# Optimization experiments

Measured on AMD Instinct MI355X. Metric: run time of the kernel, lower is better.

The kernel has to match this reference:

```python
import jax, jax.numpy as jnp
import numpy as np

DIM = 512
K_ALL = 11
K_TOP = 4
DOMAIN = 10
EPS = 1e-12
NEG_INF = -1e30

def _normalize(x):
    n = jnp.linalg.norm(x, axis=-1, keepdims=True)
    return x / jnp.maximum(n, EPS)

def _leaky(x):
    return jax.nn.leaky_relu(x, 0.01)

def setup_inputs():
    key = jax.random.key(0)
    ks = jax.random.split(key, 16)
    Bp, Lp, Bg, Lg = 128, 256, 64, 512
    probes = jax.random.normal(ks[0], (1, Bp, Lp, DIM), jnp.float32)
    gallery = jax.random.normal(ks[1], (1, Bg, Lg, DIM), jnp.float32)
    probe_lengths = jax.random.randint(ks[2], (1, Bp), 1, Lp + 1)
    gallery_lengths = jax.random.randint(ks[3], (1, Bg), 1, Lg + 1)
    proxies_p = jax.random.normal(ks[4], (K_ALL, DIM), jnp.float32) * 0.06
    proxies_g = jax.random.normal(ks[5], (K_ALL, DIM), jnp.float32) * 0.06
    transform_W = jax.random.normal(ks[6], (DOMAIN, DIM), jnp.float32) * 0.06
    transform_b = jnp.zeros((DOMAIN,), jnp.float32)
    probe_W = jnp.eye(DIM, dtype=jnp.float32)  # nn.init.eye_
    probe_b = jnp.zeros((DIM,), jnp.float32)
    # pooler MLP weights stacked over the 11 experts; init_weights: N(0, 0.001), zero bias
    pool_W1 = jax.random.normal(ks[7], (K_ALL, 2 * DIM, 3 * DIM), jnp.float32) * 1e-3
    pool_b1 = jnp.zeros((K_ALL, 2 * DIM), jnp.float32)
    pool_W2 = jax.random.normal(ks[8], (K_ALL, 2 * DIM, 2 * DIM), jnp.float32) * 1e-3
    pool_b2 = jnp.zeros((K_ALL, 2 * DIM), jnp.float32)
    pool_W3 = jax.random.normal(ks[9], (K_ALL, DIM, 2 * DIM), jnp.float32) * 1e-3
    pool_b3 = jnp.zeros((K_ALL, DIM), jnp.float32)
    return dict(probes=probes, gallery=gallery, probe_lengths=probe_lengths,
                gallery_lengths=gallery_lengths, proxies_p=proxies_p, proxies_g=proxies_g,
                transform_W=transform_W, transform_b=transform_b, probe_W=probe_W,
                probe_b=probe_b, pool_W1=pool_W1, pool_b1=pool_b1, pool_W2=pool_W2,
                pool_b2=pool_b2, pool_W3=pool_W3, pool_b3=pool_b3)

def reference(probes, gallery, probe_lengths, gallery_lengths, proxies_p, proxies_g,
              transform_W, transform_b, probe_W, probe_b,
              pool_W1, pool_b1, pool_W2, pool_b2, pool_W3, pool_b3):
    def fuse(feat, length, proxies, use_probe_linear):
        # feat: [L, D], length: scalar int; masked equivalent of feat[:length]
        L = feat.shape[0]
        fmask = (jnp.arange(L) < length).astype(feat.dtype)[:, None]  # [L, 1]
        lp = jnp.maximum(length, 1).astype(feat.dtype)
        normed = _normalize(feat)
        tf = _normalize(feat @ transform_W.T + transform_b)        # [L, 10]
        tp = _normalize(proxies @ transform_W.T + transform_b)      # [K_ALL, 10]
        sims = tf @ tp.T                                            # [L, K_ALL]
        gsim = (sims * fmask).sum(0)                                # [K_ALL]
        _, idx = jax.lax.top_k(gsim, K_TOP)
        mean = (feat * fmask).sum(0) / lp                           # [D]
        var = (((feat - mean) ** 2) * fmask).sum(0) / lp            # biased variance
        summary = jnp.concatenate([jnp.tile(mean[None], (K_TOP, 1)),
                                   jnp.tile(var[None], (K_TOP, 1)),
                                   proxies[idx]], axis=-1)          # [K_TOP, 3D]
        # expert-gathered pooler MLPs (dropout = identity in eval)
        h = _leaky(jnp.einsum('koi,ki->ko', pool_W1[idx], summary) + pool_b1[idx])
        h = _leaky(jnp.einsum('koi,ki->ko', pool_W2[idx], h) + pool_b2[idx])
        ctx = _leaky(jnp.einsum('koi,ki->ko', pool_W3[idx], h) + pool_b3[idx])  # [K_TOP, D]
        q = feat @ probe_W.T + probe_b if use_probe_linear else feat
        scores = q @ ctx.T                                          # [L, K_TOP]
        scores = jnp.where(fmask > 0, scores, NEG_INF)
        w = jax.nn.softmax(scores, axis=0)                          # softmax over set dim
        return jnp.einsum('ld,lk->kd', normed, w)                   # [K_TOP, D]

    p, g = probes[0], gallery[0]
    pl, gl = probe_lengths[0], gallery_lengths[0]
    final_probe = jax.vmap(lambda f, l: fuse(f, l, proxies_p, True))(p, pl)
    final_gallery = jax.vmap(lambda f, l: fuse(f, l, proxies_g, False))(g, gl)
    return (final_probe,
            proxies_p @ transform_W.T + transform_b,
            final_gallery,
            proxies_g @ transform_W.T + transform_b)
```

## Files before the change

### kernel.cpp

```cpp
#include <hip/hip_runtime.h>
#include <hip/hip_bf16.h>

namespace {

using us = unsigned short;
typedef __attribute__((ext_vector_type(8))) short bf16x8;
typedef __attribute__((ext_vector_type(4))) float f32x4;
typedef __attribute__((ext_vector_type(4))) unsigned short us4;
typedef __attribute__((ext_vector_type(4))) unsigned int u32x4;

constexpr int DIM_ = 512, KALL = 11, DOM = 10, NPROBE = 128, NSETS = 192;
constexpr int LPR = 256, LGA = 512;

constexpr size_t O_OUT1 = 0;
constexpr size_t O_OUT2 = (size_t)NPROBE * 4 * DIM_;
constexpr size_t O_OUT3 = O_OUT2 + KALL * DOM;
constexpr size_t O_OUT4 = O_OUT3 + (size_t)64 * 4 * DIM_;

constexpr size_t F_TP   = 64;
constexpr size_t F_IDX  = 320;
constexpr size_t F_S0A  = 1600;
constexpr size_t F_WQ   = 4096;
constexpr size_t F_GP   = 495616;
constexpr size_t F_SUMM = 514048;
constexpr size_t F_H1   = 612352;
constexpr size_t F_PART = F_H1;
constexpr size_t F_CTXW = F_H1;
constexpr size_t F_H2   = 1693696;
constexpr size_t F_ACC  = F_H2;
constexpr size_t F_CTX  = 2775040;
constexpr size_t F_WT   = 3315712;
constexpr size_t F_BEFF = 3446784;
constexpr size_t WS_FLOATS = F_BEFF + 2 * KALL * 1024;
constexpr size_t WS_BYTES  = WS_FLOATS * 4;

__device__ __forceinline__ float b2f(us u) { return __uint_as_float(((unsigned)u) << 16); }
__device__ __forceinline__ us f2b(float x) {
    unsigned u = __float_as_uint(x);
    u += 0x7FFF + ((u >> 16) & 1);
    return (us)(u >> 16);
}
__device__ __forceinline__ float ldT(const float* p) { return *p; }
__device__ __forceinline__ float ldT(const us* p) { return b2f(*p); }
__device__ __forceinline__ void stT(float* p, float v) { *p = v; }
__device__ __forceinline__ void stT(us* p, float v) { *p = f2b(v); }

__device__ __forceinline__ bf16x8 loadA(const us* p) { return *(const bf16x8*)p; }
__device__ __forceinline__ bf16x8 loadA(const float* p) {
    f32x4 a = *(const f32x4*)p, b = *(const f32x4*)(p + 4);
    bf16x8 r;
#pragma unroll
    for (int j = 0; j < 4; ++j) { r[j] = (short)f2b(a[j]); r[4 + j] = (short)f2b(b[j]); }
    return r;
}
__device__ __forceinline__ bf16x8 pack8(f32x4 a, f32x4 b) {
    bf16x8 r;
#pragma unroll
    for (int j = 0; j < 4; ++j) { r[j] = (short)f2b(a[j]); r[4 + j] = (short)f2b(b[j]); }
    return r;
}

__device__ __forceinline__ void gload_lds16(const us* g, us* l) {
    __builtin_amdgcn_global_load_lds(
        (const __attribute__((address_space(1))) void*)g,
        (__attribute__((address_space(3))) void*)l, 16, 0, 0);
}

__device__ __forceinline__ void decode64(int bx, int& set, int& base, int& L) {
    if (bx < 512) { set = bx >> 2; base = (bx & 3) * 64; L = LPR; }
    else { set = NPROBE + ((bx - 512) >> 3); base = ((bx - 512) & 7) * 64; L = LGA; }
}

__global__ void detect_kernel(const unsigned int* probeW_bits, int* flag) {
    if (threadIdx.x == 0) *flag = (probeW_bits[0] == 0x3F800000u) ? 0 : 1;
}

template <typename T>
__device__ void proxies_body(const T* pp, const T* pg, const T* tW, const T* tb,
                             float* wsf, T* dout) {
    int b = blockIdx.x;
    int fam = b / KALL, i = b % KALL;
    int lane = threadIdx.x;
    const T* src = fam ? pg : pp;
    float t[DOM];
#pragma unroll
    for (int r = 0; r < DOM; ++r) t[r] = 0.f;
    for (int d = lane; d < DIM_; d += 64) {
        float x = ldT(src + (size_t)i * DIM_ + d);
#pragma unroll
        for (int r = 0; r < DOM; ++r) t[r] += x * ldT(tW + (size_t)r * DIM_ + d);
    }
#pragma unroll
    for (int off = 32; off >= 1; off >>= 1)
#pragma unroll
        for (int r = 0; r < DOM; ++r) t[r] += __shfl_xor(t[r], off, 64);
#pragma unroll
    for (int r = 0; r < DOM; ++r) t[r] += ldT(tb + r);
    float nn = 0.f;
#pragma unroll
    for (int r = 0; r < DOM; ++r) nn += t[r] * t[r];
    float inv = 1.0f / fmaxf(sqrtf(nn), 1e-12f);
    if (lane < DOM) {
        size_t base = fam ? O_OUT4 : O_OUT2;
        stT(dout + base + i * DOM + lane, t[lane]);
        wsf[F_TP + fam * 128 + i * DOM + lane] = t[lane] * inv;
    }
}
__global__ void proxies_kernel(const int* flag, const void* pp, const void* pg,
                               const void* tW, const void* tb, float* wsf, void* dout) {
    if (*flag)
        proxies_body<us>((const us*)pp, (const us*)pg, (const us*)tW, (const us*)tb, wsf, (us*)dout);
    else
        proxies_body<float>((const float*)pp, (const float*)pg, (const float*)tW, (const float*)tb, wsf, (float*)dout);
}

template <typename T>
__device__ void pbias_body(const T* W1, const T* b1, const T* pp, const T* pg, float* beff) {
    int bx = blockIdx.x;
    int e = bx >> 4, ch = bx & 15;
    int tid = threadIdx.x;
    int om = tid >> 2, sub = tid & 3;
    int m = ch * 64 + om;
    const T* wr = W1 + ((size_t)e * 1024 + m) * 1536 + 1024 + sub * 128;
    const T* pr = pp + (size_t)e * DIM_ + sub * 128;
    const T* gr = pg + (size_t)e * DIM_ + sub * 128;
    float sp = 0.f, sg = 0.f;
    if constexpr (sizeof(T) == 2) {
#pragma unroll 4
        for (int k = 0; k < 128; k += 2) {
            unsigned wv = *(const unsigned*)(wr + k);
            unsigned pv = *(const unsigned*)(pr + k);
            unsigned gv = *(const unsigned*)(gr + k);
            float w0 = __uint_as_float(wv << 16), w1 = __uint_as_float(wv & 0xFFFF0000u);
            float p0 = __uint_as_float(pv << 16), p1 = __uint_as_float(pv & 0xFFFF0000u);
            float g0 = __uint_as_float(gv << 16), g1 = __uint_as_float(gv & 0xFFFF0000u);
            sp += w0 * p0 + w1 * p1;
            sg += w0 * g0 + w1 * g1;
        }
    } else {
#pragma unroll 2
        for (int k = 0; k < 128; k += 4) {
            f32x4 wv = *(const f32x4*)(wr + k);
            f32x4 pv = *(const f32x4*)(pr + k);
            f32x4 gv = *(const f32x4*)(gr + k);
#pragma unroll
            for (int q = 0; q < 4; ++q) { sp += wv[q] * pv[q]; sg += wv[q] * gv[q]; }
        }
    }
    sp += __shfl_xor(sp, 1, 64); sp += __shfl_xor(sp, 2, 64);
    sg += __shfl_xor(sg, 1, 64); sg += __shfl_xor(sg, 2, 64);
    if (sub == 0) {
        float bb = ldT(b1 + (size_t)e * 1024 + m);
        beff[(size_t)e * 1024 + m] = bb + sp;
        beff[(size_t)(KALL + e) * 1024 + m] = bb + sg;
    }
}
__global__ void pbias_kernel(const int* flag, const void* W1, const void* b1,
                             const void* pp, const void* pg, float* beff) {
    if (*flag)
        pbias_body<us>((const us*)W1, (const us*)b1, (const us*)pp, (const us*)pg, beff);
    else
        pbias_body<float>((const float*)W1, (const float*)b1, (const float*)pp, (const float*)pg, beff);
}

template <typename T>
__device__ void sums_body(const T* probes, const T* gallery, const int* plen,
                          const int* glen, float* wsf) {
    int bx = blockIdx.x, set = bx >> 2, c = bx & 3;
    bool probe = set < NPROBE;
    int L = probe ? LPR : LGA;
    const T* feat = probe ? probes + (size_t)set * L * DIM_
                          : gallery + (size_t)(set - NPROBE) * L * DIM_;
    int len = probe ? plen[set] : glen[set - NPROBE];
    int len_eff = min(max(len, 1), L);
    int r0 = (c * len_eff) >> 2, r1 = ((c + 1) * len_eff) >> 2;
    __shared__ float psum[DIM_], psq[DIM_];
    int tid = threadIdx.x, w = tid >> 6, lane = tid & 63;
    psum[tid] = 0.f; psum[tid + 256] = 0.f;
    psq[tid] = 0.f; psq[tid + 256] = 0.f;
    __syncthreads();
    float asum[8] = {0,0,0,0,0,0,0,0}, asq[8] = {0,0,0,0,0,0,0,0};
    for (int l = r0 + w * 2; l < r1; l += 8) {
        bool two = (l + 1 < r1);
        float f0[8], f1[8];
        if constexpr (sizeof(T) == 2) {
            u32x4 ra = *(const u32x4*)(feat + (size_t)l * DIM_ + lane * 8);
            u32x4 rb = two ? *(const u32x4*)(feat + (size_t)(l + 1) * DIM_ + lane * 8)
                           : (u32x4){0, 0, 0, 0};
#pragma unroll
            for (int q = 0; q < 4; ++q) {
                f0[2*q] = __uint_as_float(ra[q] << 16);
                f0[2*q+1] = __uint_as_float(ra[q] & 0xFFFF0000u);
                f1[2*q] = __uint_as_float(rb[q] << 16);
                f1[2*q+1] = __uint_as_float(rb[q] & 0xFFFF0000u);
            }
        } else {
            const T* rp = feat + (size_t)l * DIM_ + lane * 8;
            f32x4 a0 = *(const f32x4*)rp, a1 = *(const f32x4*)(rp + 4);
#pragma unroll
            for (int j = 0; j < 4; ++j) { f0[j] = a0[j]; f0[4+j] = a1[j]; }
            if (two) {
                const T* rq = feat + (size_t)(l + 1) * DIM_ + lane * 8;
                f32x4 b0 = *(const f32x4*)rq, b1 = *(const f32x4*)(rq + 4);
#pragma unroll
                for (int j = 0; j < 4; ++j) { f1[j] = b0[j]; f1[4+j] = b1[j]; }
            } else {
#pragma unroll
                for (int j = 0; j < 8; ++j) f1[j] = 0.f;
            }
        }
#pragma unroll
        for (int j = 0; j < 8; ++j) {
            asum[j] += f0[j] + f1[j];
            asq[j] += f0[j] * f0[j] + f1[j] * f1[j];
        }
    }
#pragma unroll
    for (int j = 0; j < 8; ++j) {
        atomicAdd(&psum[lane * 8 + j], asum[j]);
        atomicAdd(&psq[lane * 8 + j], asq[j]);
    }
    __syncthreads();
    float* P = wsf + F_PART + (size_t)bx * 1024;
    P[tid] = psum[tid]; P[tid + 256] = psum[tid + 256];
    P[512 + tid] = psq[tid]; P[768 + tid] = psq[tid + 256];
}
__global__ __launch_bounds__(256) void sums_kernel(const int* flag, const void* probes,
        const void* gallery, const int* plen, const int* glen, float* wsf) {
    if (*flag) sums_body<us>((const us*)probes, (const us*)gallery, plen, glen, wsf);
    else sums_body<float>((const float*)probes, (const float*)gallery, plen, glen, wsf);
}

template <typename T>
__device__ void sims_body(const T* probes, const T* gallery, const int* plen,
                          const int* glen, const T* tW, float* wsf) {
    int bx = blockIdx.x, set, base, L;
    decode64(bx, set, base, L);
    bool probe = set < NPROBE;
    int len = probe ? plen[set] : glen[set - NPROBE];
    int len_eff = min(max(len, 1), L);
    float* GP = wsf + F_GP + (size_t)bx * 12;
    int tid = threadIdx.x;
    if (base >= len_eff) { if (tid < KALL) GP[tid] = 0.f; return; }
    const T* feat = probe ? probes + (size_t)set * L * DIM_
                          : gallery + (size_t)(set - NPROBE) * L * DIM_;
    __shared__ __align__(16) float tile[4][320];
    __shared__ float tpl[KALL * DOM];
    __shared__ float gs[16];
    if (tid < KALL * DOM) tpl[tid] = wsf[F_TP + (probe ? 0 : 128) + tid];
    if (tid < 16) gs[tid] = 0.f;
    int w = tid >> 6, lane = tid & 63, lm = lane & 15, quad = lane >> 4;

    bf16x8 bq[16];
#pragma unroll
    for (int s = 0; s < 16; ++s) {
        if (lm < DOM) bq[s] = loadA(tW + (size_t)lm * DIM_ + s * 32 + quad * 8);
        else bq[s] = (bf16x8){0, 0, 0, 0, 0, 0, 0, 0};
    }
    int m0 = base + w * 16;
    const T* Ap = feat + (size_t)(m0 + lm) * DIM_ + quad * 8;
    f32x4 acc = (f32x4){0.f, 0.f, 0.f, 0.f};
    float vsq = 0.f;
#pragma unroll
    for (int s = 0; s < 16; ++s) {
        bf16x8 a;
        if constexpr (sizeof(T) == 2) {
            a = *(const bf16x8*)(Ap + s * 32);
#pragma unroll
            for (int j = 0; j < 8; ++j) { float x = b2f((us)a[j]); vsq += x * x; }
        } else {
            f32x4 p0 = *(const f32x4*)(Ap + s * 32), p1 = *(const f32x4*)(Ap + s * 32 + 4);
#pragma unroll
            for (int j = 0; j < 4; ++j) {
                vsq += p0[j] * p0[j] + p1[j] * p1[j];
                a[j] = (short)f2b(p0[j]); a[4 + j] = (short)f2b(p1[j]);
            }
        }
        acc = __builtin_amdgcn_mfma_f32_16x16x32_bf16(a, bq[s], acc, 0, 0, 0);
    }
    vsq += __shfl_xor(vsq, 16, 64);
    vsq += __shfl_xor(vsq, 32, 64);
    {
        int rown = m0 + lm;
        if (quad == 0 && rown < len_eff)
            wsf[F_WQ + (size_t)set * 2560 + (size_t)rown * 5 + 4] =
                1.0f / fmaxf(sqrtf(vsq), 1e-12f);
    }
#pragma unroll
    for (int r = 0; r < 4; ++r) tile[w][(quad * 4 + r) * 20 + lm] = acc[r];
    __syncthreads();

    float gacc[KALL];
#pragma unroll
    for (int k = 0; k < KALL; ++k) gacc[k] = 0.f;
    if (lane < 16) {
        int row = m0 + lane;
        if (row < len_eff) {
            const float* tr = &tile[w][lane * 20];
            f32x4 t0 = *(const f32x4*)tr, t1 = *(const f32x4*)(tr + 4);
            float tv[DOM] = {t0[0], t0[1], t0[2], t0[3], t1[0], t1[1], t1[2], t1[3], tr[8], tr[9]};
            float nn = 0.f;
#pragma unroll
            for (int r = 0; r < DOM; ++r) nn += tv[r] * tv[r];
            float inv = 1.0f / fmaxf(sqrtf(nn), 1e-12f);
#pragma unroll
            for (int k = 0; k < KALL; ++k) {
                float s = 0.f;
#pragma unroll
                for (int r = 0; r < DOM; ++r) s += tv[r] * tpl[k * DOM + r];
                gacc[k] = s * inv;
            }
        }
    }
#pragma unroll
    for (int off = 8; off >= 1; off >>= 1)
#pragma unroll
        for (int k = 0; k < KALL; ++k) gacc[k] += __shfl_xor(gacc[k], off, 64);
    if (lane == 0)
#pragma unroll
        for (int k = 0; k < KALL; ++k) atomicAdd(&gs[k], gacc[k]);
    __syncthreads();
    if (tid < KALL) GP[tid] = gs[tid];
}
__global__ __launch_bounds__(256, 3) void sims_kernel(const int* flag, const void* probes,
        const void* gallery, const int* plen, const int* glen, const void* tW, float* wsf) {
    if (*flag) sims_body<us>((const us*)probes, (const us*)gallery, plen, glen, (const us*)tW, wsf);
    else sims_body<float>((const float*)probes, (const float*)gallery, plen, glen, (const float*)tW, wsf);
}

__global__ void statsfin_kernel(const int* plen, const int* glen, float* wsf) {
    int set = blockIdx.x, tid = threadIdx.x;
    bool probe = set < NPROBE;
    int len = probe ? plen[set] : glen[set - NPROBE];
    float lp = (float)max(len, 1);
    const float* P = wsf + F_PART + (size_t)set * 4 * 1024;
    us* SUMM = (us*)(wsf + F_SUMM);
    for (int d = tid; d < DIM_; d += 256) {
        float s = P[d] + P[1024 + d] + P[2048 + d] + P[3072 + d];
        float q = P[512 + d] + P[1536 + d] + P[2560 + d] + P[3584 + d];
        float m = s / lp;
        float v = q / lp - m * m;
        SUMM[(size_t)set * 1024 + d] = f2b(m);
        SUMM[(size_t)set * 1024 + DIM_ + d] = f2b(v);
    }
    if (tid == 0) {
        int nch = probe ? 4 : 8;
        int gb = probe ? set * 4 : 512 + (set - NPROBE) * 8;
        float g[KALL];
        for (int i = 0; i < KALL; ++i) {
            float s = 0.f;
            for (int c = 0; c < nch; ++c) s += wsf[F_GP + (size_t)(gb + c) * 12 + i];
            g[i] = s;
        }
        int* idx4 = (int*)(wsf + F_IDX);
        for (int kk = 0; kk < 4; ++kk) {
            int bi = 0; float bv = g[0];
            for (int i = 1; i < KALL; ++i)
                if (g[i] > bv) { bv = g[i]; bi = i; }
            idx4[set * 4 + kk] = bi;
            g[bi] = -3e38f;
        }
    }
}

template <typename T>
__device__ void wt_body(const T* W, us* WT) {
    __shared__ us t[64][65];
    int bi = blockIdx.y * 64, bj = blockIdx.x * 64, tid = threadIdx.x;
    for (int i = tid; i < 4096; i += 256) {
        int r = i >> 6, cc = i & 63;
        t[r][cc] = (sizeof(T) == 2) ? ((const us*)W)[(size_t)(bi + r) * DIM_ + bj + cc]
                                    : f2b(ldT(W + (size_t)(bi + r) * DIM_ + bj + cc));
    }
    __syncthreads();
    for (int i = tid; i < 4096; i += 256) {
        int r = i >> 6, cc = i & 63;
        WT[(size_t)(bj + r) * DIM_ + bi + cc] = t[cc][r];
    }
}
__global__ void wt_kernel(const int* flag, const void* W, us* WT) {
    if (*flag) wt_body<us>((const us*)W, WT);
    else wt_body<float>((const float*)W, WT);
}

template <int M, int KS, int L1>
__global__ __launch_bounds__(256) void mlp_one(const int* flag, const void* Wv,
        const void* biasv, const us* X, us* Y, const float* beff) {
    constexpr int MT = M / 64;
    constexpr int NK = 16;
    int flagv = *flag;
    __shared__ us SM[8192];
    int bx = blockIdx.x;
    int nt = bx / (MT * KALL);
    int rem = bx - nt * (MT * KALL);
    int e = rem % KALL;
    int mt = rem / KALL;
    int tid = threadIdx.x, w = tid >> 6, lane = tid & 63;
    int lm = lane & 15, quad = lane >> 4;
    int s0 = nt * 64;
    const size_t aoff = ((size_t)e * M + mt * 64 + w * 16 + lm) * KS + quad * 8;
    const float* AF = (const float*)Wv + aoff;
    const us*    AB = (const us*)Wv + aoff;
    int xrow0 = (L1 ? 0 : e * NSETS) + s0;
    int slot0 = w * 64 + lane, slot1 = slot0 + 256;
    int brow0 = slot0 >> 3, bcol0 = (slot0 & 7) ^ (brow0 & 7);
    int brow1 = slot1 >> 3, bcol1 = (slot1 & 7) ^ (brow1 & 7);
    const us* Xs0 = X + ((size_t)(xrow0 + brow0)) * 1024 + bcol0 * 8;
    const us* Xs1 = X + ((size_t)(xrow0 + brow1)) * 1024 + bcol1 * 8;
    us* ls0 = SM + slot0 * 8;
    us* ls1 = SM + slot1 * 8;

    f32x4 acc[4];
#pragma unroll
    for (int j = 0; j < 4; ++j) acc[j] = (f32x4){0.f, 0.f, 0.f, 0.f};

    bf16x8 a0[2], a1[2];
    f32x4 pan[4];

    auto issueB = [&](int par, int k0) {
        gload_lds16(Xs0 + k0, ls0 + par * 4096);
        gload_lds16(Xs1 + k0, ls1 + par * 4096);
    };
    auto loadAx = [&](int k0, bf16x8* adst) {
        if (flagv) {
            adst[0] = *(const bf16x8*)(AB + k0);
            adst[1] = *(const bf16x8*)(AB + k0 + 32);
        } else {
            pan[0] = *(const f32x4*)(AF + k0);
            pan[1] = *(const f32x4*)(AF + k0 + 4);
            pan[2] = *(const f32x4*)(AF + k0 + 32);
            pan[3] = *(const f32x4*)(AF + k0 + 36);
        }
    };
    auto packA = [&](bf16x8* adst) {
        if (!flagv) {
            adst[0] = pack8(pan[0], pan[1]);
            adst[1] = pack8(pan[2], pan[3]);
        }
    };
    auto compute = [&](int par, const bf16x8* a) {
        const us* Bb = SM + par * 4096;
#pragma unroll
        for (int ks = 0; ks < 2; ++ks)
#pragma unroll
            for (int j = 0; j < 4; ++j) {
                int br = j * 16 + lm;
                int cg = ks * 4 + quad;
                bf16x8 b = *(const bf16x8*)(Bb + br * 64 + ((cg ^ (br & 7)) * 8));
                acc[j] = __builtin_amdgcn_mfma_f32_16x16x32_bf16(a[ks], b, acc[j], 0, 0, 0);
            }
    };

    issueB(0, 0);
    loadAx(0, a0);
    packA(a0);
    __syncthreads();
#pragma unroll 1
    for (int t = 0; t < NK; t += 2) {
        int k1 = (t + 1) * 64, k2 = (t + 2) * 64;
        if (t + 1 < NK) { issueB(1, k1); loadAx(k1, a1); }
        compute(0, a0);
        if (t + 1 < NK) packA(a1);
        __syncthreads();
        if (t + 1 < NK) {
            if (t + 2 < NK) { issueB(0, k2); loadAx(k2, a0); }
            compute(1, a1);
            if (t + 2 < NK) packA(a0);
            __syncthreads();
        }
    }

    int m0 = mt * 64 + w * 16 + quad * 4;
    float bv[4];
    if (L1) {
        const float* be = beff + ((size_t)((nt < 2) ? 0 : KALL) + e) * 1024 + m0;
#pragma unroll
        for (int r = 0; r < 4; ++r) bv[r] = be[r];
    } else {
#pragma unroll
        for (int r = 0; r < 4; ++r)
            bv[r] = flagv ? b2f(((const us*)biasv)[(size_t)e * M + m0 + r])
                          : ((const float*)biasv)[(size_t)e * M + m0 + r];
    }
#pragma unroll
    for (int j = 0; j < 4; ++j) {
        int s = s0 + j * 16 + lm;
        us4 pk;
#pragma unroll
        for (int r = 0; r < 4; ++r) {
            float v = acc[j][r] + bv[r];
            v = v > 0.f ? v : 0.01f * v;
            pk[r] = f2b(v);
        }
        *(us4*)(Y + ((size_t)e * NSETS + s) * M + m0) = pk;
    }
}

__global__ void fold_kernel(const us* CTX, const us* WT, us* CTXW) {
    int nt = blockIdx.x, mtb = blockIdx.y;
    int e = mtb >> 1, sub = mtb & 1;
    int row0 = e * NSETS + sub * 64;
    int tid = threadIdx.x, w = tid >> 6, lane = tid & 63;
    int lm = lane & 15, quad = lane >> 4, kq = quad * 8;
    const us* Ap = CTX + ((size_t)row0 + w * 16 + lm) * DIM_ + kq;
    int n0 = nt * 64;
    const us* Bp = WT + (size_t)(n0 + lm) * DIM_ + kq;
    f32x4 acc[4];
#pragma unroll
    for (int j = 0; j < 4; ++j) acc[j] = (f32x4){0.f, 0.f, 0.f, 0.f};
#pragma unroll 2
    for (int kc = 0; kc < DIM_; kc += 32) {
        bf16x8 a = *(const bf16x8*)(Ap + kc);
#pragma unroll
        for (int j = 0; j < 4; ++j) {
            bf16x8 b = *(const bf16x8*)(Bp + kc + (size_t)j * 16 * DIM_);
            acc[j] = __builtin_amdgcn_mfma_f32_16x16x32_bf16(a, b, acc[j], 0, 0, 0);
        }
    }
    int mrow = row0 + w * 16 + quad * 4;
#pragma unroll
    for (int j = 0; j < 4; ++j)
#pragma unroll
        for (int r = 0; r < 4; ++r)
            CTXW[(size_t)(mrow + r) * DIM_ + n0 + j * 16 + lm] = f2b(acc[j][r]);
}

template <typename T>
__device__ void s0a_body(const us* CTX, const T* pb, float* S0A) {
    int tid = threadIdx.x, w = tid >> 6, lane = tid & 63;
    int row = blockIdx.x * 4 + w;
    bf16x8 cv = *(const bf16x8*)(CTX + (size_t)row * DIM_ + lane * 8);
    float s = 0.f;
#pragma unroll
    for (int j = 0; j < 8; ++j) s += b2f((us)cv[j]) * ldT(pb + lane * 8 + j);
#pragma unroll
    for (int off = 32; off >= 1; off >>= 1) s += __shfl_xor(s, off, 64);
    if (lane == 0) S0A[row] = s;
}
__global__ void s0a_kernel(const int* flag, const us* CTX, const void* pb, float* S0A) {
    if (*flag) s0a_body<us>(CTX, (const us*)pb, S0A);
    else s0a_body<float>(CTX, (const float*)pb, S0A);
}

template <typename T>
__device__ void score_body(const T* probes, const T* gallery, const int* plen,
                           const int* glen, float* wsf) {
    int bx = blockIdx.x, set, base, L;
    decode64(bx, set, base, L);
    bool probe = set < NPROBE;
    int len = probe ? plen[set] : glen[set - NPROBE];
    int len_eff = min(max(len, 1), L);
    if (base >= len_eff) return;
    const T* feat = probe ? probes + (size_t)set * L * DIM_
                          : gallery + (size_t)(set - NPROBE) * L * DIM_;
    int tid = threadIdx.x, w = tid >> 6, lane = tid & 63;
    int lm = lane & 15, quad = lane >> 4;
    const int* idx4 = (const int*)(wsf + F_IDX);
    const us* CTXW = (const us*)(wsf + F_CTXW);
    const us* CTXR = (const us*)(wsf + F_CTX);
    bf16x8 bq[16];
    float s0v = 0.f;
    if (lm < 4) {
        int row = idx4[set * 4 + lm] * NSETS + set;
        const us* src = (probe ? CTXW : CTXR) + (size_t)row * DIM_ + quad * 8;
#pragma unroll
        for (int s = 0; s < 16; ++s) bq[s] = *(const bf16x8*)(src + s * 32);
        s0v = probe ? wsf[F_S0A + row] : 0.f;
    } else {
#pragma unroll
        for (int s = 0; s < 16; ++s) bq[s] = (bf16x8){0, 0, 0, 0, 0, 0, 0, 0};
    }
    int m0 = base + w * 16;
    const T* Ap = feat + (size_t)(m0 + lm) * DIM_ + quad * 8;
    f32x4 acc = (f32x4){0.f, 0.f, 0.f, 0.f};
#pragma unroll
    for (int s = 0; s < 16; ++s) {
        bf16x8 a = loadA(Ap + s * 32);
        acc = __builtin_amdgcn_mfma_f32_16x16x32_bf16(a, bq[s], acc, 0, 0, 0);
    }
    if (lm < 4) {
        float* wq = wsf + F_WQ + (size_t)set * 2560;
#pragma unroll
        for (int r = 0; r < 4; ++r) {
            int row = m0 + quad * 4 + r;
            wq[(size_t)row * 5 + lm] = acc[r] + s0v;
        }
    }
}
__global__ __launch_bounds__(256, 3) void score_kernel(const int* flag, const void* probes,
        const void* gallery, const int* plen, const int* glen, float* wsf) {
    if (*flag) score_body<us>((const us*)probes, (const us*)gallery, plen, glen, wsf);
    else score_body<float>((const float*)probes, (const float*)gallery, plen, glen, wsf);
}

__global__ void softmax_kernel(const int* plen, const int* glen, float* wsf) {
    int set = blockIdx.x, tid = threadIdx.x, k = tid >> 6, lane = tid & 63;
    bool probe = set < NPROBE;
    int L = probe ? LPR : LGA;
    int len = probe ? plen[set] : glen[set - NPROBE];
    int len_eff = min(max(len, 1), L);
    float* wq = wsf + F_WQ + (size_t)set * 2560;
    float cv[8];
    int n = 0;
    float m = -3e38f;
    for (int l = lane; l < len_eff; l += 64) {
        cv[n] = wq[(size_t)l * 5 + k];
        m = fmaxf(m, cv[n]);
        ++n;
    }
#pragma unroll
    for (int off = 32; off >= 1; off >>= 1) m = fmaxf(m, __shfl_xor(m, off, 64));
    float se = 0.f;
    for (int i = 0; i < n; ++i) se += __expf(cv[i] - m);
#pragma unroll
    for (int off = 32; off >= 1; off >>= 1) se += __shfl_xor(se, off, 64);
    float invs = 1.0f / se;
    n = 0;
    for (int l = lane; l < len_eff; l += 64) {
        wq[(size_t)l * 5 + k] = __expf(cv[n] - m) * invs * wq[(size_t)l * 5 + 4];
        ++n;
    }
}

template <typename T>
__device__ void accum_body(const T* probes, const T* gallery, const int* plen,
                           const int* glen, float* wsf) {
    int bx = blockIdx.x, set = bx >> 2, c = bx & 3;
    bool probe = set < NPROBE;
    int L = probe ? LPR : LGA;
    const T* feat = probe ? probes + (size_t)set * L * DIM_
                          : gallery + (size_t)(set - NPROBE) * L * DIM_;
    int len = probe ? plen[set] : glen[set - NPROBE];
    int len_eff = min(max(len, 1), L);
    int r0 = (c * len_eff) >> 2, r1 = ((c + 1) * len_eff) >> 2;
    int tid = threadIdx.x, g = tid >> 8, t = tid & 255;
    __shared__ float cf[512];
    __shared__ float pbuf[2048];
    int nr = r1 - r0;
    const float* wq = wsf + F_WQ + (size_t)set * 2560;
    for (int p = tid; p < nr * 4; p += 512)
        cf[p] = wq[(size_t)(r0 + (p >> 2)) * 5 + (p & 3)];
    __syncthreads();
    float ac[8] = {0.f, 0.f, 0.f, 0.f, 0.f, 0.f, 0.f, 0.f};
#pragma unroll 4
    for (int l = r0 + g; l < r1; l += 2) {
        float f0, f1;
        if constexpr (sizeof(T) == 2) {
            unsigned u = *(const unsigned*)((const us*)feat + (size_t)l * DIM_ + t * 2);
            f0 = __uint_as_float(u << 16);
            f1 = __uint_as_float(u & 0xFFFF0000u);
        } else {
            const T* rp = feat + (size_t)l * DIM_ + t * 2;
            f0 = rp[0]; f1 = rp[1];
        }
        f32x4 cc = *(const f32x4*)&cf[(l - r0) * 4];
#pragma unroll
        for (int k = 0; k < 4; ++k) {
            ac[k * 2] += f0 * cc[k];
            ac[k * 2 + 1] += f1 * cc[k];
        }
    }
    if (g == 1) {
#pragma unroll
        for (int i = 0; i < 8; ++i) pbuf[i * 256 + t] = ac[i];
    }
    __syncthreads();
    if (g == 0) {
        float* P = wsf + F_ACC + (size_t)bx * 2048;
#pragma unroll
        for (int k = 0; k < 4; ++k) {
            P[k * 512 + t * 2] = ac[k * 2] + pbuf[(k * 2) * 256 + t];
            P[k * 512 + t * 2 + 1] = ac[k * 2 + 1] + pbuf[(k * 2 + 1) * 256 + t];
        }
    }
}
__global__ __launch_bounds__(512) void accum_kernel(const int* flag, const void* probes,
        const void* gallery, const int* plen, const int* glen, float* wsf) {
    if (*flag) accum_body<us>((const us*)probes, (const us*)gallery, plen, glen, wsf);
    else accum_body<float>((const float*)probes, (const float*)gallery, plen, glen, wsf);
}

template <typename T>
__device__ void reduce_body(const float* wsf, T* dout) {
    int set = blockIdx.x, d = threadIdx.x;
    const float* A = wsf + F_ACC + (size_t)set * 4 * 2048;
    size_t ob = (set < NPROBE) ? O_OUT1 + (size_t)set * 2048
                               : O_OUT3 + (size_t)(set - NPROBE) * 2048;
#pragma unroll
    for (int k = 0; k < 4; ++k) {
        float s = A[k * 512 + d] + A[2048 + k * 512 + d] + A[4096 + k * 512 + d] + A[6144 + k * 512 + d];
        stT(dout + ob + k * 512 + d, s);
    }
}
__global__ __launch_bounds__(512) void reduce_kernel(const int* flag, const float* wsf, void* dout) {
    if (*flag) reduce_body<us>(wsf, (us*)dout);
    else reduce_body<float>(wsf, (float*)dout);
}

}

extern "C" void kernel_launch(void* const* d_in, const int* in_sizes, int n_in,
                              void* d_out, int out_size, void* d_ws, size_t ws_size,
                              hipStream_t stream) {
    if (ws_size < WS_BYTES) return;
    float* wsf = (float*)d_ws;
    int* flag = (int*)d_ws;
    us* SUMM = (us*)(wsf + F_SUMM);
    us* H1 = (us*)(wsf + F_H1);
    us* H2 = (us*)(wsf + F_H2);
    us* CTXb = (us*)(wsf + F_CTX);
    us* CTXW = (us*)(wsf + F_CTXW);
    us* WT = (us*)(wsf + F_WT);
    const int* plen = (const int*)d_in[2];
    const int* glen = (const int*)d_in[3];

    detect_kernel<<<1, 64, 0, stream>>>((const unsigned int*)d_in[8], flag);
    proxies_kernel<<<22, 64, 0, stream>>>(flag, d_in[4], d_in[5], d_in[6], d_in[7], wsf, d_out);
    pbias_kernel<<<176, 256, 0, stream>>>(flag, d_in[10], d_in[11], d_in[4], d_in[5], wsf + F_BEFF);
    wt_kernel<<<dim3(8, 8), 256, 0, stream>>>(flag, d_in[8], WT);
    sums_kernel<<<NSETS * 4, 256, 0, stream>>>(flag, d_in[0], d_in[1], plen, glen, wsf);
    sims_kernel<<<1024, 256, 0, stream>>>(flag, d_in[0], d_in[1], plen, glen, d_in[6], wsf);
    statsfin_kernel<<<NSETS, 256, 0, stream>>>(plen, glen, wsf);

    mlp_one<1024, 1536, 1><<<3 * 16 * KALL, 256, 0, stream>>>(
        flag, d_in[10], nullptr, SUMM, H1, wsf + F_BEFF);
    mlp_one<1024, 1024, 0><<<3 * 16 * KALL, 256, 0, stream>>>(
        flag, d_in[12], d_in[13], H1, H2, nullptr);
    mlp_one<512, 1024, 0><<<3 * 8 * KALL, 256, 0, stream>>>(
        flag, d_in[14], d_in[15], H2, CTXb, nullptr);

    fold_kernel<<<dim3(8, 22), 256, 0, stream>>>(CTXb, WT, CTXW);
    s0a_kernel<<<528, 256, 0, stream>>>(flag, CTXb, d_in[9], wsf + F_S0A);
    score_kernel<<<1024, 256, 0, stream>>>(flag, d_in[0], d_in[1], plen, glen, wsf);
    softmax_kernel<<<NSETS, 256, 0, stream>>>(plen, glen, wsf);
    accum_kernel<<<NSETS * 4, 512, 0, stream>>>(flag, d_in[0], d_in[1], plen, glen, wsf);
    reduce_kernel<<<NSETS, 512, 0, stream>>>(flag, wsf, d_out);
}
```

Measured before the change: 429.5 us.

## Fuse per-set sum/sumsq statistics into the similarity kernel's 64-row chunks

Removes the separate sums kernel and computes per-feature sum and sum-of-squares inside sims_kernel over each block's 64-row chunk, writing per-chunk partials that statsfin now reduces over 4 or 8 chunks. This avoids a second full read of probes and gallery and one kernel launch. In exchange, sims_kernel uses more shared memory and adds work before its MFMA section, which may lower occupancy under its launch bounds. The partial buffer layout now grows to 1024 chunks, so the F_PART region has to be large enough to hold them.

Measured after the change: 430.5 us. Within noise of the previous version (+0.2%).

```diff
diff --git a/kernel.cpp b/kernel.cpp
--- a/kernel.cpp
+++ b/kernel.cpp
@@ -164,74 +164,6 @@
 }
 
 template <typename T>
-__device__ void sums_body(const T* probes, const T* gallery, const int* plen,
-                          const int* glen, float* wsf) {
-    int bx = blockIdx.x, set = bx >> 2, c = bx & 3;
-    bool probe = set < NPROBE;
-    int L = probe ? LPR : LGA;
-    const T* feat = probe ? probes + (size_t)set * L * DIM_
-                          : gallery + (size_t)(set - NPROBE) * L * DIM_;
-    int len = probe ? plen[set] : glen[set - NPROBE];
-    int len_eff = min(max(len, 1), L);
-    int r0 = (c * len_eff) >> 2, r1 = ((c + 1) * len_eff) >> 2;
-    __shared__ float psum[DIM_], psq[DIM_];
-    int tid = threadIdx.x, w = tid >> 6, lane = tid & 63;
-    psum[tid] = 0.f; psum[tid + 256] = 0.f;
-    psq[tid] = 0.f; psq[tid + 256] = 0.f;
-    __syncthreads();
-    float asum[8] = {0,0,0,0,0,0,0,0}, asq[8] = {0,0,0,0,0,0,0,0};
-    for (int l = r0 + w * 2; l < r1; l += 8) {
-        bool two = (l + 1 < r1);
-        float f0[8], f1[8];
-        if constexpr (sizeof(T) == 2) {
-            u32x4 ra = *(const u32x4*)(feat + (size_t)l * DIM_ + lane * 8);
-            u32x4 rb = two ? *(const u32x4*)(feat + (size_t)(l + 1) * DIM_ + lane * 8)
-                           : (u32x4){0, 0, 0, 0};
-#pragma unroll
-            for (int q = 0; q < 4; ++q) {
-                f0[2*q] = __uint_as_float(ra[q] << 16);
-                f0[2*q+1] = __uint_as_float(ra[q] & 0xFFFF0000u);
-                f1[2*q] = __uint_as_float(rb[q] << 16);
-                f1[2*q+1] = __uint_as_float(rb[q] & 0xFFFF0000u);
-            }
-        } else {
-            const T* rp = feat + (size_t)l * DIM_ + lane * 8;
-            f32x4 a0 = *(const f32x4*)rp, a1 = *(const f32x4*)(rp + 4);
-#pragma unroll
-            for (int j = 0; j < 4; ++j) { f0[j] = a0[j]; f0[4+j] = a1[j]; }
-            if (two) {
-                const T* rq = feat + (size_t)(l + 1) * DIM_ + lane * 8;
-                f32x4 b0 = *(const f32x4*)rq, b1 = *(const f32x4*)(rq + 4);
-#pragma unroll
-                for (int j = 0; j < 4; ++j) { f1[j] = b0[j]; f1[4+j] = b1[j]; }
-            } else {
-#pragma unroll
-                for (int j = 0; j < 8; ++j) f1[j] = 0.f;
-            }
-        }
-#pragma unroll
-        for (int j = 0; j < 8; ++j) {
-            asum[j] += f0[j] + f1[j];
-            asq[j] += f0[j] * f0[j] + f1[j] * f1[j];
-        }
-    }
-#pragma unroll
-    for (int j = 0; j < 8; ++j) {
-        atomicAdd(&psum[lane * 8 + j], asum[j]);
-        atomicAdd(&psq[lane * 8 + j], asq[j]);
-    }
-    __syncthreads();
-    float* P = wsf + F_PART + (size_t)bx * 1024;
-    P[tid] = psum[tid]; P[tid + 256] = psum[tid + 256];
-    P[512 + tid] = psq[tid]; P[768 + tid] = psq[tid + 256];
-}
-__global__ __launch_bounds__(256) void sums_kernel(const int* flag, const void* probes,
-        const void* gallery, const int* plen, const int* glen, float* wsf) {
-    if (*flag) sums_body<us>((const us*)probes, (const us*)gallery, plen, glen, wsf);
-    else sums_body<float>((const float*)probes, (const float*)gallery, plen, glen, wsf);
-}
-
-template <typename T>
 __device__ void sims_body(const T* probes, const T* gallery, const int* plen,
                           const int* glen, const T* tW, float* wsf) {
     int bx = blockIdx.x, set, base, L;
@@ -240,16 +172,77 @@
     int len = probe ? plen[set] : glen[set - NPROBE];
     int len_eff = min(max(len, 1), L);
     float* GP = wsf + F_GP + (size_t)bx * 12;
+    float* PART = wsf + F_PART + (size_t)bx * 1024;
     int tid = threadIdx.x;
-    if (base >= len_eff) { if (tid < KALL) GP[tid] = 0.f; return; }
+    int nvalid = len_eff - base;
+    if (nvalid <= 0) {
+        if (tid < KALL) GP[tid] = 0.f;
+        for (int d = tid; d < 1024; d += 256) PART[d] = 0.f;
+        return;
+    }
+    nvalid = min(nvalid, 64);
     const T* feat = probe ? probes + (size_t)set * L * DIM_
                           : gallery + (size_t)(set - NPROBE) * L * DIM_;
     __shared__ __align__(16) float tile[4][320];
     __shared__ float tpl[KALL * DOM];
     __shared__ float gs[16];
+    __shared__ float psum[DIM_], psq[DIM_];
     if (tid < KALL * DOM) tpl[tid] = wsf[F_TP + (probe ? 0 : 128) + tid];
     if (tid < 16) gs[tid] = 0.f;
+    psum[tid] = 0.f; psum[tid + 256] = 0.f;
+    psq[tid] = 0.f; psq[tid + 256] = 0.f;
+    __syncthreads();
+
     int w = tid >> 6, lane = tid & 63, lm = lane & 15, quad = lane >> 4;
+
+    {
+        int cl = lane;
+        const T* fb = feat + (size_t)base * DIM_ + cl * 8;
+        float asum[8] = {0,0,0,0,0,0,0,0}, asq[8] = {0,0,0,0,0,0,0,0};
+        for (int r = w; r < nvalid; r += 8) {
+            bool two = (r + 4 < nvalid);
+            float f0[8], f1[8];
+            if constexpr (sizeof(T) == 2) {
+                u32x4 ra = *(const u32x4*)(fb + (size_t)r * DIM_);
+                u32x4 rb = two ? *(const u32x4*)(fb + (size_t)(r + 4) * DIM_)
+                               : (u32x4){0, 0, 0, 0};
+#pragma unroll
+                for (int q = 0; q < 4; ++q) {
+                    f0[2*q]   = __uint_as_float(ra[q] << 16);
+                    f0[2*q+1] = __uint_as_float(ra[q] & 0xFFFF0000u);
+                    f1[2*q]   = __uint_as_float(rb[q] << 16);
+                    f1[2*q+1] = __uint_as_float(rb[q] & 0xFFFF0000u);
+                }
+            } else {
+                const T* rp = fb + (size_t)r * DIM_;
+                f32x4 a0 = *(const f32x4*)rp, a1 = *(const f32x4*)(rp + 4);
+#pragma unroll
+                for (int j = 0; j < 4; ++j) { f0[j] = a0[j]; f0[4+j] = a1[j]; }
+                if (two) {
+                    const T* rq = fb + (size_t)(r + 4) * DIM_;
+                    f32x4 b0 = *(const f32x4*)rq, b1 = *(const f32x4*)(rq + 4);
+#pragma unroll
+                    for (int j = 0; j < 4; ++j) { f1[j] = b0[j]; f1[4+j] = b1[j]; }
+                } else {
+#pragma unroll
+                    for (int j = 0; j < 8; ++j) f1[j] = 0.f;
+                }
+            }
+#pragma unroll
+            for (int j = 0; j < 8; ++j) {
+                asum[j] += f0[j] + f1[j];
+                asq[j] += f0[j] * f0[j] + f1[j] * f1[j];
+            }
+        }
+#pragma unroll
+        for (int j = 0; j < 8; ++j) {
+            atomicAdd(&psum[cl * 8 + j], asum[j]);
+            atomicAdd(&psq[cl * 8 + j], asq[j]);
+        }
+    }
+    __syncthreads();
+    PART[tid] = psum[tid]; PART[tid + 256] = psum[tid + 256];
+    PART[512 + tid] = psq[tid]; PART[768 + tid] = psq[tid + 256];
 
     bf16x8 bq[16];
 #pragma unroll
@@ -333,18 +326,22 @@
     bool probe = set < NPROBE;
     int len = probe ? plen[set] : glen[set - NPROBE];
     float lp = (float)max(len, 1);
-    const float* P = wsf + F_PART + (size_t)set * 4 * 1024;
+    int nch = probe ? 4 : 8;
+    int cb = probe ? set * 4 : 512 + (set - NPROBE) * 8;
+    const float* P = wsf + F_PART + (size_t)cb * 1024;
     us* SUMM = (us*)(wsf + F_SUMM);
     for (int d = tid; d < DIM_; d += 256) {
-        float s = P[d] + P[1024 + d] + P[2048 + d] + P[3072 + d];
-        float q = P[512 + d] + P[1536 + d] + P[2560 + d] + P[3584 + d];
+        float s = 0.f, q = 0.f;
+        for (int c = 0; c < nch; ++c) {
+            s += P[(size_t)c * 1024 + d];
+            q += P[(size_t)c * 1024 + 512 + d];
+        }
         float m = s / lp;
         float v = q / lp - m * m;
         SUMM[(size_t)set * 1024 + d] = f2b(m);
         SUMM[(size_t)set * 1024 + DIM_ + d] = f2b(v);
     }
     if (tid == 0) {
-        int nch = probe ? 4 : 8;
         int gb = probe ? set * 4 : 512 + (set - NPROBE) * 8;
         float g[KALL];
         for (int i = 0; i < KALL; ++i) {
@@ -718,7 +715,6 @@
     proxies_kernel<<<22, 64, 0, stream>>>(flag, d_in[4], d_in[5], d_in[6], d_in[7], wsf, d_out);
     pbias_kernel<<<176, 256, 0, stream>>>(flag, d_in[10], d_in[11], d_in[4], d_in[5], wsf + F_BEFF);
     wt_kernel<<<dim3(8, 8), 256, 0, stream>>>(flag, d_in[8], WT);
-    sums_kernel<<<NSETS * 4, 256, 0, stream>>>(flag, d_in[0], d_in[1], plen, glen, wsf);
     sims_kernel<<<1024, 256, 0, stream>>>(flag, d_in[0], d_in[1], plen, glen, d_in[6], wsf);
     statsfin_kernel<<<NSETS, 256, 0, stream>>>(plen, glen, wsf);
 
```
